# Optimization experiments

Measured on AMD Instinct MI355X. Metric: run time of the kernel, lower is better.

The kernel has to match this reference:

```python
import jax, jax.numpy as jnp
import numpy as np

B, N_IN, N_OUT, C = 4, 512, 1024, 64
INIT_LENGTH_SCALE = 0.1


def setup_inputs() -> dict:
    key = jax.random.key(0)
    k1, k2, k3, k4, k5 = jax.random.split(key, 5)
    x = jax.random.uniform(k1, (B, N_IN, 1), dtype=jnp.float32)
    y = jax.random.normal(k2, (B, N_IN, C), dtype=jnp.float32)
    t = jax.random.uniform(k3, (B, N_OUT, 1), dtype=jnp.float32)
    # learnable params: per-channel log length-scale, pointwise linear C -> 1
    sigma = jnp.full((C,), np.log(INIT_LENGTH_SCALE), dtype=jnp.float32)
    w = jax.random.normal(k4, (C, 1), dtype=jnp.float32) / np.sqrt(C)
    b = jnp.zeros((1,), dtype=jnp.float32)
    return {"x": x, "y": y, "t": t, "sigma": sigma, "w": w, "b": b}


def reference(x, y, t, sigma, w, b):
    # pairwise squared distances: (B, n_in, n_out)
    dists = (x - jnp.swapaxes(t, 1, 2)) ** 2
    scales = jnp.exp(sigma)  # (C,)
    # RBF weights, broadcast over channels: (B, n_in, n_out, C)
    wt = jnp.exp(-0.5 * dists[..., None] / scales**2)
    # weighted sum over input points: (B, n_out, C)
    y_out = jnp.einsum("bnc,bnmc->bmc", y, wt)
    # pointwise linear C -> 1: (B, n_out, 1)
    return y_out @ w + b
```

## Files before the change

kernel.cpp:

```cpp
#include <hip/hip_runtime.h>

constexpr int Bb   = 4;
constexpr int NIN  = 512;
constexpr int NOUT = 1024;
constexpr int CC   = 64;

constexpr int MTILE = 16;

__global__ __launch_bounds__(256) void rbf_fused(
    const float* __restrict__ x,     const float* __restrict__ y,
    const float* __restrict__ t,     const float* __restrict__ sigma,
    const float* __restrict__ w,     const float* __restrict__ bias,
    float* __restrict__ out)
{
    __shared__ float xs[NIN];
    __shared__ float yt[NIN];
    __shared__ float part[64];

    const int tid  = threadIdx.x;
    const int lane = tid & 63;
    const int g    = tid >> 6;
    const int mt   = blockIdx.x & (NOUT / MTILE - 1);
    const int b    = blockIdx.x >> 6;

    const float s0  = sigma[0];
    const bool  uni = (__ballot(sigma[lane] == s0) == ~0ull);

    if (uni) {
        const float s = 0.84932180f * __expf(-s0);

        xs[tid]       = x[b * NIN + tid]       * s;
        xs[tid + 256] = x[b * NIN + tid + 256] * s;

        const int    r  = lane >> 4;
        const int    cg = lane & 15;
        const float4 wv = ((const float4*)w)[cg];
        const float4* __restrict__ y4 = (const float4*)(y + (size_t)b * NIN * CC);
#pragma unroll 4
        for (int it = 0; it < NIN / 16; ++it) {
            const int n = g * (NIN / 4) + it * 4 + r;
            const float4 v = y4[n * (CC / 4) + cg];
            float p = v.x * wv.x + v.y * wv.y + v.z * wv.z + v.w * wv.w;
            p += __shfl_xor(p, 1, 64);
            p += __shfl_xor(p, 2, 64);
            p += __shfl_xor(p, 4, 64);
            p += __shfl_xor(p, 8, 64);
            if (cg == 0) yt[n] = p;
        }
        __syncthreads();

        const int msub = lane >> 2;
        const int nsub = g * 4 + (lane & 3);
        const int m    = mt * MTILE + msub;
        const float tm = t[b * NOUT + m] * s;
        float a0 = 0.f, a1 = 0.f, a2 = 0.f, a3 = 0.f;
#pragma unroll
        for (int k = 0; k < 32; k += 4) {
            const int n0 = nsub + 16 * k;
            const float d0 = xs[n0]      - tm;
            const float d1 = xs[n0 + 16] - tm;
            const float d2 = xs[n0 + 32] - tm;
            const float d3 = xs[n0 + 48] - tm;
            a0 += __builtin_amdgcn_exp2f(-(d0 * d0)) * yt[n0];
            a1 += __builtin_amdgcn_exp2f(-(d1 * d1)) * yt[n0 + 16];
            a2 += __builtin_amdgcn_exp2f(-(d2 * d2)) * yt[n0 + 32];
            a3 += __builtin_amdgcn_exp2f(-(d3 * d3)) * yt[n0 + 48];
        }
        float acc = (a0 + a1) + (a2 + a3);
        acc += __shfl_xor(acc, 1, 64);
        acc += __shfl_xor(acc, 2, 64);
        if ((lane & 3) == 0) part[g * 16 + msub] = acc;
        __syncthreads();
        if (tid < 16) {
            const float rsum = (part[tid] + part[16 + tid]) +
                               (part[32 + tid] + part[48 + tid]) + bias[0];
            out[b * NOUT + mt * MTILE + tid] = rsum;
        }
    } else {
        const float kc2 = -0.72134752f * __expf(-2.0f * sigma[lane]);
        const float wc  = w[lane];
        const float* __restrict__ xb = x + b * NIN;
        const float* __restrict__ yb = y + (size_t)b * NIN * CC + lane;
        for (int j = 0; j < 4; ++j) {
            const int   mm = mt * MTILE + g * 4 + j;
            const float tm = t[b * NOUT + mm];
            float acc = 0.f;
            for (int n = 0; n < NIN; ++n) {
                const float d = xb[n] - tm;
                acc += __builtin_amdgcn_exp2f(d * d * kc2) * yb[(size_t)n * CC];
            }
            float p = acc * wc;
#pragma unroll
            for (int off = 32; off > 0; off >>= 1) p += __shfl_xor(p, off, 64);
            if (lane == 0) out[b * NOUT + mm] = p + bias[0];
        }
    }
}

extern "C" void kernel_launch(void* const* d_in, const int* in_sizes, int n_in,
                              void* d_out, int out_size, void* d_ws, size_t ws_size,
                              hipStream_t stream) {
    const float* x     = (const float*)d_in[0];
    const float* y     = (const float*)d_in[1];
    const float* t     = (const float*)d_in[2];
    const float* sigma = (const float*)d_in[3];
    const float* w     = (const float*)d_in[4];
    const float* bias  = (const float*)d_in[5];
    float* out = (float*)d_out;
    (void)d_ws; (void)ws_size;

    rbf_fused<<<Bb * (NOUT / MTILE), 256, 0, stream>>>(x, y, t, sigma, w, bias, out);
}
```

Measured before the change: 76.23 us.

## Enlarge output tile to 64 per block with 8 waves and per-lane outputs

Result: faster. 71.92 us (-5.7%).

```diff
diff --git a/kernel.cpp b/kernel.cpp
--- a/kernel.cpp
+++ b/kernel.cpp
@@ -5,9 +5,10 @@
 constexpr int NOUT = 1024;
 constexpr int CC   = 64;
 
-constexpr int MTILE = 16;
+constexpr int MTILE = 64;
+constexpr int NW    = 8;
 
-__global__ __launch_bounds__(256) void rbf_fused(
+__global__ __launch_bounds__(512) void rbf_fused(
     const float* __restrict__ x,     const float* __restrict__ y,
     const float* __restrict__ t,     const float* __restrict__ sigma,
     const float* __restrict__ w,     const float* __restrict__ bias,
@@ -15,13 +16,13 @@
 {
     __shared__ float xs[NIN];
     __shared__ float yt[NIN];
-    __shared__ float part[64];
+    __shared__ float part[NW * 64];
 
     const int tid  = threadIdx.x;
     const int lane = tid & 63;
     const int g    = tid >> 6;
     const int mt   = blockIdx.x & (NOUT / MTILE - 1);
-    const int b    = blockIdx.x >> 6;
+    const int b    = blockIdx.x >> 4;
 
     const float s0  = sigma[0];
     const bool  uni = (__ballot(sigma[lane] == s0) == ~0ull);
@@ -29,16 +30,15 @@
     if (uni) {
         const float s = 0.84932180f * __expf(-s0);
 
-        xs[tid]       = x[b * NIN + tid]       * s;
-        xs[tid + 256] = x[b * NIN + tid + 256] * s;
+        if (tid < NIN) xs[tid] = x[b * NIN + tid] * s;
 
         const int    r  = lane >> 4;
         const int    cg = lane & 15;
         const float4 wv = ((const float4*)w)[cg];
         const float4* __restrict__ y4 = (const float4*)(y + (size_t)b * NIN * CC);
 #pragma unroll 4
-        for (int it = 0; it < NIN / 16; ++it) {
-            const int n = g * (NIN / 4) + it * 4 + r;
+        for (int it = 0; it < 16; ++it) {
+            const int n = g * 64 + it * 4 + r;
             const float4 v = y4[n * (CC / 4) + cg];
             float p = v.x * wv.x + v.y * wv.y + v.z * wv.z + v.w * wv.w;
             p += __shfl_xor(p, 1, 64);
@@ -49,40 +49,38 @@
         }
         __syncthreads();
 
-        const int msub = lane >> 2;
-        const int nsub = g * 4 + (lane & 3);
-        const int m    = mt * MTILE + msub;
+        const int   m  = mt * MTILE + lane;
         const float tm = t[b * NOUT + m] * s;
+        const float* __restrict__ xg = xs + g * 64;
+        const float* __restrict__ yg = yt + g * 64;
         float a0 = 0.f, a1 = 0.f, a2 = 0.f, a3 = 0.f;
-#pragma unroll
-        for (int k = 0; k < 32; k += 4) {
-            const int n0 = nsub + 16 * k;
-            const float d0 = xs[n0]      - tm;
-            const float d1 = xs[n0 + 16] - tm;
-            const float d2 = xs[n0 + 32] - tm;
-            const float d3 = xs[n0 + 48] - tm;
-            a0 += __builtin_amdgcn_exp2f(-(d0 * d0)) * yt[n0];
-            a1 += __builtin_amdgcn_exp2f(-(d1 * d1)) * yt[n0 + 16];
-            a2 += __builtin_amdgcn_exp2f(-(d2 * d2)) * yt[n0 + 32];
-            a3 += __builtin_amdgcn_exp2f(-(d3 * d3)) * yt[n0 + 48];
+#pragma unroll 4
+        for (int n = 0; n < 64; n += 4) {
+            const float d0 = xg[n + 0] - tm;
+            const float d1 = xg[n + 1] - tm;
+            const float d2 = xg[n + 2] - tm;
+            const float d3 = xg[n + 3] - tm;
+            a0 += __builtin_amdgcn_exp2f(-(d0 * d0)) * yg[n + 0];
+            a1 += __builtin_amdgcn_exp2f(-(d1 * d1)) * yg[n + 1];
+            a2 += __builtin_amdgcn_exp2f(-(d2 * d2)) * yg[n + 2];
+            a3 += __builtin_amdgcn_exp2f(-(d3 * d3)) * yg[n + 3];
         }
-        float acc = (a0 + a1) + (a2 + a3);
-        acc += __shfl_xor(acc, 1, 64);
-        acc += __shfl_xor(acc, 2, 64);
-        if ((lane & 3) == 0) part[g * 16 + msub] = acc;
+        part[g * 64 + lane] = (a0 + a1) + (a2 + a3);
         __syncthreads();
-        if (tid < 16) {
-            const float rsum = (part[tid] + part[16 + tid]) +
-                               (part[32 + tid] + part[48 + tid]) + bias[0];
-            out[b * NOUT + mt * MTILE + tid] = rsum;
+        if (g == 0) {
+            const float rsum = ((part[lane]       + part[64 + lane]) +
+                                (part[128 + lane] + part[192 + lane])) +
+                               ((part[256 + lane] + part[320 + lane]) +
+                                (part[384 + lane] + part[448 + lane])) + bias[0];
+            out[b * NOUT + m] = rsum;
         }
     } else {
         const float kc2 = -0.72134752f * __expf(-2.0f * sigma[lane]);
         const float wc  = w[lane];
         const float* __restrict__ xb = x + b * NIN;
         const float* __restrict__ yb = y + (size_t)b * NIN * CC + lane;
-        for (int j = 0; j < 4; ++j) {
-            const int   mm = mt * MTILE + g * 4 + j;
+        for (int j = 0; j < 8; ++j) {
+            const int   mm = mt * MTILE + g * 8 + j;
             const float tm = t[b * NOUT + mm];
             float acc = 0.f;
             for (int n = 0; n < NIN; ++n) {
@@ -109,5 +107,5 @@
     float* out = (float*)d_out;
     (void)d_ws; (void)ws_size;
 
-    rbf_fused<<<Bb * (NOUT / MTILE), 256, 0, stream>>>(x, y, t, sigma, w, bias, out);
+    rbf_fused<<<Bb * (NOUT / MTILE), 512, 0, stream>>>(x, y, t, sigma, w, bias, out);
 }
```
